# Kernel optimization log

Measured on AMD Instinct MI355X. Metric: run time of the kernel, lower is better.

The kernel has to match this reference:

```python
import jax, jax.numpy as jnp
import numpy as np

B, N, D, H, L, R = 2, 1024, 128, 8, 8, 4
HD = D // H            # head dim = 16
DH = int(D * 2.0)      # mlp hidden (mlp_ratio=2.0)
TWO_R = 2 * R
LS_INIT = 1e-3


def _ln(x, g, b):
    m = x.mean(-1, keepdims=True)
    v = ((x - m) ** 2).mean(-1, keepdims=True)
    return (x - m) / jnp.sqrt(v + 1e-5) * g + b


def _gelu(t):
    return jax.nn.gelu(t, approximate=False)  # torch nn.GELU default (erf)


def _attn(x, mask, bias, qkv_w, proj_w, proj_b, w_pre, w_post):
    Bx, Nx, C = x.shape
    qkv = (x @ qkv_w.T).reshape(Bx, Nx, 3, H, HD).transpose(2, 0, 3, 1, 4)
    q, k, v = qkv[0], qkv[1], qkv[2]               # each [B,H,N,hd]
    a = jnp.einsum('bhid,bhjd->bhij', q, k) * (HD ** -0.5)
    a = a + mask[:, None] + bias                   # pairwise mask + rbf/edge bias
    a = jnp.einsum('bhij,gh->bgij', a, w_pre)      # talk-head pre-softmax
    a = jax.nn.softmax(a, axis=-1)
    a = jnp.einsum('bhij,gh->bgij', a, w_post)     # talk-head post-softmax
    o = jnp.einsum('bhij,bhjd->bihd', a, v).reshape(Bx, Nx, C)
    return o @ proj_w.T + proj_b


def setup_inputs() -> dict:
    key = jax.random.key(0)
    ks = jax.random.split(key, 16)
    s = 0.02
    x = jax.random.normal(ks[0], (B, N, D), jnp.float32)
    dist = jax.random.uniform(ks[1], (B, N, N), jnp.float32) * 20.0
    attn_mask = jnp.where(jax.random.uniform(ks[2], (B, N, N)) < 0.02, -1e4, 0.0).astype(jnp.float32)
    local_mask = jnp.where(dist > 8.0, -1e4, 0.0).astype(jnp.float32)
    edge_type = jax.random.randint(ks[3], (B, N, N), 0, 4)
    return {
        'x': x, 'dist': dist, 'attn_mask': attn_mask, 'local_mask': local_mask,
        'edge_type': edge_type,
        'ln_g': jnp.ones((L, 3, D), jnp.float32), 'ln_b': jnp.zeros((L, 3, D), jnp.float32),
        'qkv_w': jax.random.normal(ks[4], (L, 2, 3 * D, D), jnp.float32) * s,
        'proj_w': jax.random.normal(ks[5], (L, 2, D, D), jnp.float32) * s,
        'proj_b': jnp.zeros((L, 2, D), jnp.float32),
        'th_pre': jnp.eye(H, dtype=jnp.float32) + jax.random.normal(ks[6], (L, 2, H, H), jnp.float32) * s,
        'th_post': jnp.eye(H, dtype=jnp.float32) + jax.random.normal(ks[7], (L, 2, H, H), jnp.float32) * s,
        'ls': jnp.full((L, 3, D), LS_INIT, jnp.float32),
        'fc1_w': jax.random.normal(ks[8], (L, DH, D), jnp.float32) * s,
        'fc1_b': jnp.zeros((L, DH), jnp.float32),
        'fc2_w': jax.random.normal(ks[9], (L, D, DH), jnp.float32) * s,
        'fc2_b': jnp.zeros((L, D), jnp.float32),
        'de_ln_g': jnp.ones((L, TWO_R), jnp.float32), 'de_ln_b': jnp.zeros((L, TWO_R), jnp.float32),
        'de_w': jax.random.normal(ks[10], (L, H, TWO_R), jnp.float32) * 0.5,
        'de_b': jnp.zeros((L, H), jnp.float32),
        'edge_emb': jax.random.normal(ks[11], (L, 4, R), jnp.float32) * 0.5,
        'rbf_mu': jnp.linspace(0.0, 20.0, R).astype(jnp.float32),
        'rbf_sigma': jnp.full((R,), 20.0 / R, jnp.float32),
    }


def reference(x, dist, attn_mask, local_mask, edge_type, ln_g, ln_b, qkv_w, proj_w,
              proj_b, th_pre, th_post, ls, fc1_w, fc1_b, fc2_w, fc2_b,
              de_ln_g, de_ln_b, de_w, de_b, edge_emb, rbf_mu, rbf_sigma):
    # RBF features of pairwise distances: [B,N,N,R] (mu/sigma buffers shared across layers)
    rbf = jnp.exp(-(((dist[..., None] - rbf_mu) / rbf_sigma) ** 2))
    first_mask = attn_mask + local_mask  # num_dist_mask == 1
    for l in range(L):
        feat = jnp.concatenate([rbf, edge_emb[l][edge_type]], axis=-1)  # [B,N,N,2R]
        bias = _gelu(_ln(feat, de_ln_g[l], de_ln_b[l]) @ de_w[l].T + de_b[l])  # [B,N,N,H]
        bias = jnp.moveaxis(bias, -1, 1)  # [B,H,N,N]
        x = x + ls[l, 0] * _attn(_ln(x, ln_g[l, 0], ln_b[l, 0]), first_mask, bias,
                                 qkv_w[l, 0], proj_w[l, 0], proj_b[l, 0], th_pre[l, 0], th_post[l, 0])
        x = x + ls[l, 1] * _attn(_ln(x, ln_g[l, 1], ln_b[l, 1]), attn_mask, bias,
                                 qkv_w[l, 1], proj_w[l, 1], proj_b[l, 1], th_pre[l, 1], th_post[l, 1])
        h = _ln(x, ln_g[l, 2], ln_b[l, 2])
        h = _gelu(h @ fc1_w[l].T + fc1_b[l]) @ fc2_w[l].T + fc2_b[l]
        x = x + ls[l, 2] * h
    return x
```

## Files before the change

kernel.cpp:

```cpp
#include <hip/hip_runtime.h>
#include <math.h>

#define BB 2
#define NN 1024
#define DD 128
#define HH 8
#define NL 8
#define RR 4
#define DHID 256
#define TWO_R 8
#define MM (BB*NN)
#define TB 2048

typedef __attribute__((ext_vector_type(8))) short short8;
typedef __attribute__((ext_vector_type(4))) float f32x4;

__device__ __forceinline__ float gelu_erf(float x) {
    return 0.5f * x * (1.0f + erff(x * 0.70710678118654752f));
}
__device__ __forceinline__ ushort f2b(float f) {
    union { float f; unsigned u; } v; v.f = f;
    return (ushort)((v.u + 0x7FFFu + ((v.u >> 16) & 1u)) >> 16);
}
__device__ __forceinline__ float b2f(ushort u) {
    union { unsigned u; float f; } v; v.u = ((unsigned)u) << 16;
    return v.f;
}
__device__ __forceinline__ unsigned pk2(float a, float b) {
    return ((unsigned)f2b(b) << 16) | (unsigned)f2b(a);
}

__global__ __launch_bounds__(256) void cvt4_kernel(
    const float* __restrict__ s0, int n0, const float* __restrict__ s1, int n1,
    const float* __restrict__ s2, int n2, const float* __restrict__ s3, int n3,
    ushort* __restrict__ d0, ushort* __restrict__ d1,
    ushort* __restrict__ d2, ushort* __restrict__ d3) {
    int t = blockIdx.x * 256 + threadIdx.x;
    if (t < n0) { d0[t] = f2b(s0[t]); return; } t -= n0;
    if (t < n1) { d1[t] = f2b(s1[t]); return; } t -= n1;
    if (t < n2) { d2[t] = f2b(s2[t]); return; } t -= n2;
    if (t < n3) { d3[t] = f2b(s3[t]); }
}

__global__ __launch_bounds__(256) void maskprep_kernel(
    const float* __restrict__ am, const float* __restrict__ lm,
    ushort* __restrict__ fmask, ushort* __restrict__ amask) {
    int t = blockIdx.x * 256 + threadIdx.x;
    if (t >= BB * NN * NN) return;
    float a = am[t];
    amask[t] = f2b(a);
    fmask[t] = f2b(a + lm[t]);
}

__global__ __launch_bounds__(256) void table_kernel(
    const float* __restrict__ de_ln_g, const float* __restrict__ de_ln_b,
    const float* __restrict__ de_w, const float* __restrict__ de_b,
    const float* __restrict__ edge_emb, const float* __restrict__ mu,
    const float* __restrict__ sigma, float* __restrict__ tab) {
    int t = blockIdx.x * 256 + threadIdx.x;
    if (t >= NL * 4 * TB) return;
    int idx = t & (TB - 1);
    int et = (t >> 11) & 3;
    int l = t >> 13;
    float d = idx * (20.0f / (float)(TB - 1));
    float f[8];
#pragma unroll
    for (int r = 0; r < RR; ++r) {
        float u = (d - mu[r]) / sigma[r];
        f[r] = expf(-u * u);
    }
#pragma unroll
    for (int r = 0; r < RR; ++r) f[4 + r] = edge_emb[(l * 4 + et) * RR + r];
    float m = 0.f;
#pragma unroll
    for (int r = 0; r < 8; ++r) m += f[r];
    m *= 0.125f;
    float v = 0.f;
#pragma unroll
    for (int r = 0; r < 8; ++r) { float dd = f[r] - m; v += dd * dd; }
    v *= 0.125f;
    float inv = rsqrtf(v + 1e-5f);
    float fn[8];
#pragma unroll
    for (int r = 0; r < 8; ++r)
        fn[r] = (f[r] - m) * inv * de_ln_g[l * 8 + r] + de_ln_b[l * 8 + r];
#pragma unroll
    for (int h = 0; h < HH; ++h) {
        float z = de_b[l * 8 + h];
#pragma unroll
        for (int r = 0; r < 8; ++r) z += de_w[(l * 8 + h) * 8 + r] * fn[r];
        tab[(size_t)t * 8 + h] = gelu_erf(z);
    }
}

#define GF_BIAS 1
#define GF_GELU 2
#define GF_RESID 4
#define GF_OUTBF 8

template <int AMODE, int FLAGS, int KDIM>
__global__ __launch_bounds__(256) void gemm_mfma(
    const void* __restrict__ Ain, const ushort* __restrict__ W,
    const float* __restrict__ bias, const float* __restrict__ ls,
    const float* __restrict__ resid, const float* __restrict__ lng,
    const float* __restrict__ lnb, void* __restrict__ out, int Nd) {
    __shared__ ushort As[64][KDIM + 8];
    __shared__ ushort Ws[64][KDIM + 8];
    int tid = threadIdx.x;
    int bm = blockIdx.x, bn = blockIdx.y;
    if (AMODE == 1) {
        int r = tid >> 2, c = tid & 3;
        const float* xr = (const float*)Ain + (size_t)(bm * 64 + r) * 128 + c * 32;
        float v[32];
        float s = 0.f, ss = 0.f;
#pragma unroll
        for (int k = 0; k < 8; ++k) {
            float4 f = ((const float4*)xr)[k];
            v[4 * k] = f.x; v[4 * k + 1] = f.y; v[4 * k + 2] = f.z; v[4 * k + 3] = f.w;
            s += f.x + f.y + f.z + f.w;
            ss += f.x * f.x + f.y * f.y + f.z * f.z + f.w * f.w;
        }
        s += __shfl_xor(s, 1, 64);  s += __shfl_xor(s, 2, 64);
        ss += __shfl_xor(ss, 1, 64); ss += __shfl_xor(ss, 2, 64);
        float mean = s * (1.f / 128.f);
        float var = ss * (1.f / 128.f) - mean * mean;
        float inv = rsqrtf(var + 1e-5f);
        unsigned* dst = (unsigned*)&As[r][c * 32];
#pragma unroll
        for (int k = 0; k < 16; ++k) {
            int col = c * 32 + 2 * k;
            float a0 = (v[2 * k] - mean) * inv * lng[col] + lnb[col];
            float a1 = (v[2 * k + 1] - mean) * inv * lng[col + 1] + lnb[col + 1];
            dst[k] = pk2(a0, a1);
        }
    } else if (AMODE == 2) {
        const float* Apart = (const float*)Ain;
        for (int v = tid; v < 64 * 32; v += 256) {
            int r = v >> 5, c = v & 31;
            size_t off = (size_t)(bm * 64 + r) * 128 + c * 4;
            float4 s0 = *(const float4*)(Apart + off);
            float4 s1 = *(const float4*)(Apart + (size_t)MM * 128 + off);
            unsigned* dst = (unsigned*)&As[r][c * 4];
            dst[0] = pk2(s0.x + s1.x, s0.y + s1.y);
            dst[1] = pk2(s0.z + s1.z, s0.w + s1.w);
        }
    } else {
        const ushort* A = (const ushort*)Ain;
        for (int v = tid; v < 64 * KDIM / 8; v += 256) {
            int r = v / (KDIM / 8), c = v % (KDIM / 8);
            *(short8*)&As[r][c * 8] =
                *(const short8*)(A + (size_t)(bm * 64 + r) * KDIM + c * 8);
        }
    }
    for (int v = tid; v < 64 * KDIM / 8; v += 256) {
        int r = v / (KDIM / 8), c = v % (KDIM / 8);
        *(short8*)&Ws[r][c * 8] =
            *(const short8*)(W + (size_t)(bn * 64 + r) * KDIM + c * 8);
    }
    __syncthreads();
    int wv = tid >> 6, l = tid & 63;
    int wm = (wv >> 1) * 32, wn = (wv & 1) * 32;
    int lr = l & 15, lk = (l >> 4) * 8;
    f32x4 acc[2][2] = {};
#pragma unroll
    for (int k0 = 0; k0 < KDIM; k0 += 32) {
        short8 af[2], bf[2];
        af[0] = *(const short8*)&As[wm + lr][k0 + lk];
        af[1] = *(const short8*)&As[wm + 16 + lr][k0 + lk];
        bf[0] = *(const short8*)&Ws[wn + lr][k0 + lk];
        bf[1] = *(const short8*)&Ws[wn + 16 + lr][k0 + lk];
#pragma unroll
        for (int mf = 0; mf < 2; ++mf)
#pragma unroll
            for (int nf = 0; nf < 2; ++nf)
                acc[mf][nf] = __builtin_amdgcn_mfma_f32_16x16x32_bf16(
                    af[mf], bf[nf], acc[mf][nf], 0, 0, 0);
    }
#pragma unroll
    for (int mf = 0; mf < 2; ++mf)
#pragma unroll
        for (int nf = 0; nf < 2; ++nf) {
            int n = bn * 64 + wn + nf * 16 + lr;
            float bv = (FLAGS & GF_BIAS) ? bias[n] : 0.f;
            float lv = (FLAGS & GF_RESID) ? ls[n] : 0.f;
#pragma unroll
            for (int q = 0; q < 4; ++q) {
                int m = bm * 64 + wm + mf * 16 + (l >> 4) * 4 + q;
                float c = acc[mf][nf][q];
                c += bv;
                if (FLAGS & GF_GELU) c = gelu_erf(c);
                size_t idx = (size_t)m * Nd + n;
                if (FLAGS & GF_RESID) c = resid[idx] + lv * c;
                if (FLAGS & GF_OUTBF) ((ushort*)out)[idx] = f2b(c);
                else ((float*)out)[idx] = c;
            }
        }
}

__global__ __launch_bounds__(256) void score_mfma(
    const ushort* __restrict__ qkv, const float* __restrict__ dist,
    const int* __restrict__ edge_type, const float* __restrict__ tabl,
    const ushort* __restrict__ mask, ushort* __restrict__ a) {
    int tid = threadIdx.x, wv = tid >> 6, l = tid & 63;
    int jt = blockIdx.x, it = blockIdx.y, b = blockIdx.z;
    int i0 = it * 16, j0 = jt * 64;
    int h0 = wv * 2;
    int lr = l & 15, kk = (l >> 4) * 8;
    short8 zero = {0, 0, 0, 0, 0, 0, 0, 0};
    bool lo = kk < 16;
    short8 af[2];
    short8 bf[2][4];
    f32x4 acc[2][4] = {};
#pragma unroll
    for (int hh = 0; hh < 2; ++hh) {
        af[hh] = zero;
        if (lo)
            af[hh] = *(const short8*)(qkv + (size_t)(b * NN + i0 + lr) * 384 +
                                      (h0 + hh) * 16 + kk);
#pragma unroll
        for (int nf = 0; nf < 4; ++nf) {
            bf[hh][nf] = zero;
            if (lo)
                bf[hh][nf] = *(const short8*)(qkv +
                                              (size_t)(b * NN + j0 + nf * 16 + lr) * 384 +
                                              128 + (h0 + hh) * 16 + kk);
        }
    }
#pragma unroll
    for (int hh = 0; hh < 2; ++hh)
#pragma unroll
        for (int nf = 0; nf < 4; ++nf)
            acc[hh][nf] = __builtin_amdgcn_mfma_f32_16x16x32_bf16(
                af[hh], bf[hh][nf], acc[hh][nf], 0, 0, 0);
#pragma unroll
    for (int nf = 0; nf < 4; ++nf)
#pragma unroll
        for (int q = 0; q < 4; ++q) {
            int i = i0 + (l >> 4) * 4 + q;
            int j = j0 + nf * 16 + lr;
            size_t mi = ((size_t)b * NN + i) * NN + j;
            float d = dist[mi];
            int et = edge_type[mi];
            float msk = b2f(mask[mi]);
            float u = d * ((float)(TB - 1) / 20.0f);
            int t0i = (int)u;
            t0i = t0i < 0 ? 0 : (t0i > TB - 2 ? TB - 2 : t0i);
            float fr = u - (float)t0i;
            const float* tp = tabl + ((size_t)et * TB + t0i) * 8 + h0;
            float2 lo2 = *(const float2*)tp;
            float2 hi2 = *(const float2*)(tp + 8);
            float bv0 = lo2.x + fr * (hi2.x - lo2.x);
            float bv1 = lo2.y + fr * (hi2.y - lo2.y);
            size_t ai0 = ((size_t)(b * HH + h0) * NN + i) * NN + j;
            a[ai0] = f2b(acc[0][nf][q] * 0.25f + msk + bv0);
            a[ai0 + (size_t)NN * NN] = f2b(acc[1][nf][q] * 0.25f + msk + bv1);
        }
}

__global__ __launch_bounds__(256) void mixsm_kernel(
    ushort* __restrict__ a, const float* __restrict__ pre,
    const float* __restrict__ post) {
    __shared__ float red[8][4];
    int bi = blockIdx.x;
    int b = bi >> 10, i = bi & 1023;
    int tid = threadIdx.x, wave = tid >> 6, lane = tid & 63;
    float vals[8][4];
#pragma unroll
    for (int h = 0; h < HH; ++h) {
        uint2 w = *(const uint2*)(a + ((size_t)(b * HH + h) * NN + i) * NN + 4 * tid);
        vals[h][0] = b2f((ushort)(w.x & 0xFFFF));
        vals[h][1] = b2f((ushort)(w.x >> 16));
        vals[h][2] = b2f((ushort)(w.y & 0xFFFF));
        vals[h][3] = b2f((ushort)(w.y >> 16));
    }
    float e[8][4];
#pragma unroll
    for (int g = 0; g < HH; ++g) {
        float pr[8];
#pragma unroll
        for (int h = 0; h < 8; ++h) pr[h] = pre[g * 8 + h];
        float z = 0.f;
#pragma unroll
        for (int q = 0; q < 4; ++q) {
            float m = 0.f;
#pragma unroll
            for (int h = 0; h < 8; ++h) m += pr[h] * vals[h][q];
            e[g][q] = __expf(m);
            z += e[g][q];
        }
#pragma unroll
        for (int o = 32; o; o >>= 1) z += __shfl_xor(z, o, 64);
        if (lane == 0) red[g][wave] = z;
    }
    __syncthreads();
#pragma unroll
    for (int g = 0; g < HH; ++g) {
        float rz = 1.f / (red[g][0] + red[g][1] + red[g][2] + red[g][3]);
#pragma unroll
        for (int q = 0; q < 4; ++q) e[g][q] *= rz;
    }
#pragma unroll
    for (int g = 0; g < HH; ++g) {
        float po[8];
#pragma unroll
        for (int h = 0; h < 8; ++h) po[h] = post[g * 8 + h];
        float o4[4];
#pragma unroll
        for (int q = 0; q < 4; ++q) {
            float s = 0.f;
#pragma unroll
            for (int h = 0; h < 8; ++h) s += po[h] * e[h][q];
            o4[q] = s;
        }
        uint2 w;
        w.x = pk2(o4[0], o4[1]);
        w.y = pk2(o4[2], o4[3]);
        *(uint2*)(a + ((size_t)(b * HH + g) * NN + i) * NN + 4 * tid) = w;
    }
}

__global__ __launch_bounds__(256) void av_mfma(
    const ushort* __restrict__ p, const ushort* __restrict__ qkv,
    float* __restrict__ opart) {
    __shared__ ushort Vs[16][520];
    int bx = blockIdx.x;
    int it = bx >> 1, js = bx & 1;
    int bh = blockIdx.y;
    int b = bh >> 3, h = bh & 7;
    int tid = threadIdx.x, wv = tid >> 6, l = tid & 63;
    int i0 = it * 64 + wv * 16;
    int j0 = js * 512;
    for (int jl = tid; jl < 512; jl += 256) {
        const ushort* src = qkv + (size_t)(b * NN + j0 + jl) * 384 + 256 + h * 16;
        short8 v0 = *(const short8*)src;
        short8 v1 = *(const short8*)(src + 8);
#pragma unroll
        for (int d = 0; d < 8; ++d) Vs[d][jl] = (ushort)v0[d];
#pragma unroll
        for (int d = 0; d < 8; ++d) Vs[8 + d][jl] = (ushort)v1[d];
    }
    __syncthreads();
    int lr = l & 15, lk = (l >> 4) * 8;
    const ushort* prow = p + ((size_t)bh * NN + i0 + lr) * NN + j0;
    f32x4 acc0 = {}, acc1 = {};
#pragma unroll
    for (int ks = 0; ks < 16; ks += 2) {
        int jb0 = ks * 32 + lk;
        int jb1 = (ks + 1) * 32 + lk;
        short8 bv0 = *(const short8*)&Vs[lr][jb0];
        short8 bv1 = *(const short8*)&Vs[lr][jb1];
        short8 a0 = *(const short8*)(prow + jb0);
        short8 a1 = *(const short8*)(prow + jb1);
        acc0 = __builtin_amdgcn_mfma_f32_16x16x32_bf16(a0, bv0, acc0, 0, 0, 0);
        acc1 = __builtin_amdgcn_mfma_f32_16x16x32_bf16(a1, bv1, acc1, 0, 0, 0);
    }
    f32x4 acc = acc0 + acc1;
#pragma unroll
    for (int q = 0; q < 4; ++q) {
        int m = i0 + (l >> 4) * 4 + q;
        opart[((size_t)js * MM + b * NN + m) * DD + h * 16 + lr] = acc[q];
    }
}

extern "C" void kernel_launch(void* const* d_in, const int* in_sizes, int n_in,
                              void* d_out, int out_size, void* d_ws, size_t ws_size,
                              hipStream_t stream) {
    const float* x         = (const float*)d_in[0];
    const float* dist      = (const float*)d_in[1];
    const float* attn_mask = (const float*)d_in[2];
    const float* local_mask= (const float*)d_in[3];
    const int*   edge_type = (const int*)d_in[4];
    const float* ln_g      = (const float*)d_in[5];
    const float* ln_b      = (const float*)d_in[6];
    const float* qkv_w     = (const float*)d_in[7];
    const float* proj_w    = (const float*)d_in[8];
    const float* proj_b    = (const float*)d_in[9];
    const float* th_pre    = (const float*)d_in[10];
    const float* th_post   = (const float*)d_in[11];
    const float* ls        = (const float*)d_in[12];
    const float* fc1_w     = (const float*)d_in[13];
    const float* fc1_b     = (const float*)d_in[14];
    const float* fc2_w     = (const float*)d_in[15];
    const float* fc2_b     = (const float*)d_in[16];
    const float* de_ln_g   = (const float*)d_in[17];
    const float* de_ln_b   = (const float*)d_in[18];
    const float* de_w      = (const float*)d_in[19];
    const float* de_b      = (const float*)d_in[20];
    const float* edge_emb  = (const float*)d_in[21];
    const float* rbf_mu    = (const float*)d_in[22];
    const float* rbf_sigma = (const float*)d_in[23];

    char* pws = (char*)d_ws;
    auto alloc = [&](size_t bytes) {
        char* r = pws;
        pws += (bytes + 255) & ~(size_t)255;
        return (void*)r;
    };
    const int NWQ = NL * 2 * 3 * DD * DD;
    const int NWP = NL * 2 * DD * DD;
    const int NW1 = NL * DHID * DD;
    const int NW2 = NL * DD * DHID;
    ushort* wq    = (ushort*)alloc((size_t)NWQ * 2);
    ushort* wp    = (ushort*)alloc((size_t)NWP * 2);
    ushort* w1    = (ushort*)alloc((size_t)NW1 * 2);
    ushort* w2    = (ushort*)alloc((size_t)NW2 * 2);
    ushort* abuf  = (ushort*)alloc((size_t)BB * HH * NN * NN * 2);
    ushort* fmask = (ushort*)alloc((size_t)BB * NN * NN * 2);
    ushort* amask = (ushort*)alloc((size_t)BB * NN * NN * 2);
    float*  xbuf  = (float*)alloc((size_t)MM * DD * 4);
    ushort* qkvb  = (ushort*)alloc((size_t)MM * 3 * DD * 2);
    ushort* h1    = (ushort*)alloc((size_t)MM * DHID * 2);
    float*  opart = (float*)alloc((size_t)2 * MM * DD * 4);
    float*  tab   = (float*)alloc((size_t)NL * 4 * TB * 8 * 4);

    {
        int ntot = NWQ + NWP + NW1 + NW2;
        cvt4_kernel<<<(ntot + 255) / 256, 256, 0, stream>>>(
            qkv_w, NWQ, proj_w, NWP, fc1_w, NW1, fc2_w, NW2, wq, wp, w1, w2);
        maskprep_kernel<<<(BB * NN * NN + 255) / 256, 256, 0, stream>>>(
            attn_mask, local_mask, fmask, amask);
        table_kernel<<<(NL * 4 * TB + 255) / 256, 256, 0, stream>>>(
            de_ln_g, de_ln_b, de_w, de_b, edge_emb, rbf_mu, rbf_sigma, tab);
    }

    hipMemcpyAsync(xbuf, x, (size_t)MM * DD * 4, hipMemcpyDeviceToDevice, stream);

    for (int l = 0; l < NL; ++l) {
        const float* tabl = tab + (size_t)l * 4 * TB * 8;
        for (int inst = 0; inst < 2; ++inst) {
            gemm_mfma<1, GF_OUTBF, 128><<<dim3(MM / 64, 384 / 64), 256, 0, stream>>>(
                xbuf, wq + (size_t)(l * 2 + inst) * 3 * DD * DD,
                nullptr, nullptr, nullptr,
                ln_g + (l * 3 + inst) * DD, ln_b + (l * 3 + inst) * DD, qkvb, 384);
            score_mfma<<<dim3(NN / 64, NN / 16, BB), 256, 0, stream>>>(
                qkvb, dist, edge_type, tabl, inst == 0 ? fmask : amask, abuf);
            mixsm_kernel<<<BB * NN, 256, 0, stream>>>(
                abuf, th_pre + (l * 2 + inst) * HH * HH,
                th_post + (l * 2 + inst) * HH * HH);
            av_mfma<<<dim3(32, BB * HH), 256, 0, stream>>>(abuf, qkvb, opart);
            gemm_mfma<2, GF_BIAS | GF_RESID, 128>
                <<<dim3(MM / 64, DD / 64), 256, 0, stream>>>(
                opart, wp + (size_t)(l * 2 + inst) * DD * DD,
                proj_b + (l * 2 + inst) * DD, ls + (l * 3 + inst) * DD,
                xbuf, nullptr, nullptr, xbuf, DD);
        }

        gemm_mfma<1, GF_BIAS | GF_GELU | GF_OUTBF, 128>
            <<<dim3(MM / 64, DHID / 64), 256, 0, stream>>>(
            xbuf, w1 + (size_t)l * DHID * DD, fc1_b + l * DHID,
            nullptr, nullptr, ln_g + (l * 3 + 2) * DD, ln_b + (l * 3 + 2) * DD,
            h1, DHID);
        gemm_mfma<0, GF_BIAS | GF_RESID, 256>
            <<<dim3(MM / 64, DD / 64), 256, 0, stream>>>(
            h1, w2 + (size_t)l * DD * DHID, fc2_b + l * DD,
            ls + (l * 3 + 2) * DD, xbuf, nullptr, nullptr, xbuf, DD);
    }

    hipMemcpyAsync(d_out, xbuf, (size_t)MM * DD * 4, hipMemcpyDeviceToDevice, stream);
}
```

Measured before the change: 1.529 ms.

## Deduplicate bias loads and stage score tile in LDS for coalesced stores

The score kernel now loads dist, edge_type and mask once per pair with vector loads, computes the interpolated bias for all heads, and keeps bias plus mask in shared memory as packed bf16. The outputs are staged in an LDS tile and written with 16-byte coalesced stores instead of scattered 2-byte stores. This removes fourfold redundant global reads and uncoalesced writes, at the cost of LDS use, two barriers, and an extra bf16 rounding of the bias.

```diff
diff --git a/kernel.cpp b/kernel.cpp
--- a/kernel.cpp
+++ b/kernel.cpp
@@ -201,9 +201,51 @@
     const ushort* __restrict__ qkv, const float* __restrict__ dist,
     const int* __restrict__ edge_type, const float* __restrict__ tabl,
     const ushort* __restrict__ mask, ushort* __restrict__ a) {
+    __shared__ unsigned bm2[4][1024];
+    __shared__ ushort st[8][16][72];
     int tid = threadIdx.x, wv = tid >> 6, l = tid & 63;
     int jt = blockIdx.x, it = blockIdx.y, b = blockIdx.z;
     int i0 = it * 16, j0 = jt * 64;
+    {
+        int p0 = tid * 4;
+        int il = p0 >> 6, jl = p0 & 63;
+        size_t mi = ((size_t)(b * NN + i0 + il)) * NN + j0 + jl;
+        float4 d4 = *(const float4*)(dist + mi);
+        int4 e4 = *(const int4*)(edge_type + mi);
+        uint2 mk = *(const uint2*)(mask + mi);
+        float mk4[4] = { b2f((ushort)(mk.x & 0xFFFF)), b2f((ushort)(mk.x >> 16)),
+                         b2f((ushort)(mk.y & 0xFFFF)), b2f((ushort)(mk.y >> 16)) };
+        float dv[4] = { d4.x, d4.y, d4.z, d4.w };
+        int ev[4] = { e4.x, e4.y, e4.z, e4.w };
+        unsigned o[4][4];
+#pragma unroll
+        for (int p = 0; p < 4; ++p) {
+            float u = dv[p] * ((float)(TB - 1) / 20.0f);
+            int t0i = (int)u;
+            t0i = t0i < 0 ? 0 : (t0i > TB - 2 ? TB - 2 : t0i);
+            float fr = u - (float)t0i;
+            const float* tp = tabl + ((size_t)ev[p] * TB + t0i) * 8;
+            float4 lo0 = *(const float4*)tp;
+            float4 lo1 = *(const float4*)(tp + 4);
+            float4 hi0 = *(const float4*)(tp + 8);
+            float4 hi1 = *(const float4*)(tp + 12);
+            float m = mk4[p];
+            o[p][0] = pk2(m + lo0.x + fr * (hi0.x - lo0.x),
+                          m + lo0.y + fr * (hi0.y - lo0.y));
+            o[p][1] = pk2(m + lo0.z + fr * (hi0.z - lo0.z),
+                          m + lo0.w + fr * (hi0.w - lo0.w));
+            o[p][2] = pk2(m + lo1.x + fr * (hi1.x - lo1.x),
+                          m + lo1.y + fr * (hi1.y - lo1.y));
+            o[p][3] = pk2(m + lo1.z + fr * (hi1.z - lo1.z),
+                          m + lo1.w + fr * (hi1.w - lo1.w));
+        }
+#pragma unroll
+        for (int hp = 0; hp < 4; ++hp) {
+            uint4 w4;
+            w4.x = o[0][hp]; w4.y = o[1][hp]; w4.z = o[2][hp]; w4.w = o[3][hp];
+            *reinterpret_cast<uint4*>(&bm2[hp][p0]) = w4;
+        }
+    }
     int h0 = wv * 2;
     int lr = l & 15, kk = (l >> 4) * 8;
     short8 zero = {0, 0, 0, 0, 0, 0, 0, 0};
@@ -232,29 +274,29 @@
         for (int nf = 0; nf < 4; ++nf)
             acc[hh][nf] = __builtin_amdgcn_mfma_f32_16x16x32_bf16(
                 af[hh], bf[hh][nf], acc[hh][nf], 0, 0, 0);
+    __syncthreads();
 #pragma unroll
     for (int nf = 0; nf < 4; ++nf)
 #pragma unroll
         for (int q = 0; q < 4; ++q) {
-            int i = i0 + (l >> 4) * 4 + q;
-            int j = j0 + nf * 16 + lr;
-            size_t mi = ((size_t)b * NN + i) * NN + j;
-            float d = dist[mi];
-            int et = edge_type[mi];
-            float msk = b2f(mask[mi]);
-            float u = d * ((float)(TB - 1) / 20.0f);
-            int t0i = (int)u;
-            t0i = t0i < 0 ? 0 : (t0i > TB - 2 ? TB - 2 : t0i);
-            float fr = u - (float)t0i;
-            const float* tp = tabl + ((size_t)et * TB + t0i) * 8 + h0;
-            float2 lo2 = *(const float2*)tp;
-            float2 hi2 = *(const float2*)(tp + 8);
-            float bv0 = lo2.x + fr * (hi2.x - lo2.x);
-            float bv1 = lo2.y + fr * (hi2.y - lo2.y);
-            size_t ai0 = ((size_t)(b * HH + h0) * NN + i) * NN + j;
-            a[ai0] = f2b(acc[0][nf][q] * 0.25f + msk + bv0);
-            a[ai0 + (size_t)NN * NN] = f2b(acc[1][nf][q] * 0.25f + msk + bv1);
-        }
+            int il = (l >> 4) * 4 + q;
+            int jl = nf * 16 + lr;
+            unsigned bmv = bm2[wv][il * 64 + jl];
+            st[h0][il][jl]     = f2b(acc[0][nf][q] * 0.25f + b2f((ushort)(bmv & 0xFFFF)));
+            st[h0 + 1][il][jl] = f2b(acc[1][nf][q] * 0.25f + b2f((ushort)(bmv >> 16)));
+        }
+    __syncthreads();
+    {
+        int row = tid >> 1;
+        int h = row >> 4, il = row & 15;
+        int jl = (tid & 1) * 32;
+        const ushort* src = &st[h][il][jl];
+        ushort* dst = a + ((size_t)(b * HH + h) * NN + i0 + il) * NN + j0 + jl;
+        *reinterpret_cast<uint4*>(dst)      = *reinterpret_cast<const uint4*>(src);
+        *reinterpret_cast<uint4*>(dst + 8)  = *reinterpret_cast<const uint4*>(src + 8);
+        *reinterpret_cast<uint4*>(dst + 16) = *reinterpret_cast<const uint4*>(src + 16);
+        *reinterpret_cast<uint4*>(dst + 24) = *reinterpret_cast<const uint4*>(src + 24);
+    }
 }
 
 __global__ __launch_bounds__(256) void mixsm_kernel(
```

Result: faster. 1.426 ms (-6.8%).
